# Kernel tuning notes

Hardware: AMD Instinct MI355X
Metric: run time of the kernel (lower is better)

## Reference

```python
import jax, jax.numpy as jnp
import numpy as np

L, E, K, H, I = 2, 8, 2, 1024, 2048  # stack_size, num_experts, top_k, hidden, intermediate
B, S = 1, 2048


def setup_inputs() -> dict:
    key = jax.random.key(0)
    k0, k1, k2, k3 = jax.random.split(key, 4)
    hidden_states = jax.random.normal(k0, (B, S, H), dtype=jnp.float32)
    router_w = jax.random.normal(k1, (L, H, E), dtype=jnp.float32) * 0.02
    gate_up_proj = jax.random.normal(k2, (L, E, H, 2 * I), dtype=jnp.float32) * (1.0 / np.sqrt(H))
    down_proj = jax.random.normal(k3, (L, E, I, H), dtype=jnp.float32) * (1.0 / np.sqrt(I))
    return {"hidden_states": hidden_states, "router_w": router_w,
            "gate_up_proj": gate_up_proj, "down_proj": down_proj}


def _moe_layer(x, rw, gu_w, dn_w):
    # x: [T,H]; one MoE block: RouterTopK(softmax) + full-capacity top-k GLU expert MLPs
    logits = x @ rw                                   # [T,E] router linear (fp32)
    aff = jax.nn.softmax(logits, axis=-1)
    vals, idx = jax.lax.top_k(aff, K)                 # [T,K]
    vals = vals / jnp.sum(vals, axis=-1, keepdims=True)  # normalize_top_k_affinities=True
    T = x.shape[0]
    # sparse combine weights [T,E]: normalized affinity on chosen experts, 0 elsewhere
    combine = jnp.zeros((T, E), x.dtype).at[jnp.arange(T)[:, None], idx].set(vals)
    gu = jnp.einsum('th,ehi->eti', x, gu_w)           # [E,T,2I] fused gate+up per expert
    gate, up = gu[..., :I], gu[..., I:]
    act = jax.nn.silu(gate) * up                      # GLU with silu
    eo = jnp.einsum('eti,eih->eth', act, dn_w)        # [E,T,H] down proj
    out = jnp.einsum('eth,te->th', eo, combine)       # combine over experts
    return out, logits


def reference(hidden_states, router_w, gate_up_proj, down_proj):
    Bx, Sx, Hx = hidden_states.shape
    x = hidden_states.reshape(-1, Hx)                 # [T,H]
    logits_all = []
    for l in range(L):                                # fixed small stack of layers
        x, logits = _moe_layer(x, router_w[l], gate_up_proj[l], down_proj[l])
        logits_all.append(logits)
    return x.reshape(Bx, Sx, Hx), jnp.stack(logits_all)  # output, [L,T,E] router logits
```

## Files before the change

kernel.cpp:

```cpp
#include <hip/hip_runtime.h>
#include <cstdint>
#include <cstddef>

constexpr int Lc = 2, Ec = 8, Hc = 1024, Ic = 2048, Tc = 2048;

typedef __bf16 bf16x8 __attribute__((ext_vector_type(8)));
typedef float f32x4 __attribute__((ext_vector_type(4)));

__device__ __forceinline__ unsigned short f2bf(float f) {
  unsigned u = __builtin_bit_cast(unsigned, f);
  u = (u + 0x7fffu + ((u >> 16) & 1u)) >> 16;
  return (unsigned short)u;
}
__device__ __forceinline__ float bf2f(unsigned short h) {
  unsigned u = (unsigned)h << 16;
  return __builtin_bit_cast(float, u);
}
__device__ __forceinline__ bf16x8 ldfrag(const unsigned short* p) {
  return __builtin_bit_cast(bf16x8, *(const uint4*)p);
}

template <bool WSPLIT>
__device__ __forceinline__ void wconv_block(const float* __restrict__ src,
                                            unsigned short* __restrict__ dh,
                                            unsigned short* __restrict__ dl,
                                            int K, int N, int idx, char* smem) {
  const int nN = N >> 6, nK = K >> 6;
  const int sN = 31 - __builtin_clz((unsigned)nN);
  const int sK = 31 - __builtin_clz((unsigned)nK);
  const int bx = idx & (nN - 1);
  const int by = (idx >> sN) & (nK - 1);
  const int e = idx >> (sN + sK);
  const int n0 = bx * 64, k0 = by * 64;
  const int NB = N >> 6, KS = K >> 5;
  src += (size_t)e * K * N;

  unsigned short(*lh)[66] = (unsigned short(*)[66])smem;
  unsigned short(*ll)[66] = (unsigned short(*)[66])(smem + 64 * 66 * 2);
  const int tid = threadIdx.x;

  {
    const int r = tid >> 2, cg = (tid & 3) * 16;
    const float* sp = src + (size_t)(k0 + r) * N + n0 + cg;
#pragma unroll
    for (int i = 0; i < 16; i += 4) {
      const float4 v = *(const float4*)(sp + i);
      const float f[4] = {v.x, v.y, v.z, v.w};
#pragma unroll
      for (int j = 0; j < 4; ++j) {
        const unsigned short h = f2bf(f[j]);
        lh[r][cg + i + j] = h;
        if constexpr (WSPLIT) ll[r][cg + i + j] = f2bf(f[j] - bf2f(h));
      }
    }
  }
  __syncthreads();
  {
    const int ksl = tid >> 7, q = (tid >> 5) & 3, n2 = (tid & 31) * 2;
    const int kb = ksl * 32 + q * 8;
    union { unsigned short s[16]; uint4 u[2]; } oh, ol;
#pragma unroll
    for (int s = 0; s < 2; ++s)
#pragma unroll
      for (int i = 0; i < 8; ++i) {
        oh.s[s * 8 + i] = lh[kb + i][n2 + s];
        if constexpr (WSPLIT) ol.s[s * 8 + i] = ll[kb + i][n2 + s];
      }
    const size_t cb =
        (((size_t)e * NB + (n0 >> 6)) * KS + (k0 >> 5) + ksl) * 2048 + q * 512 + n2 * 8;
    *(uint4*)(dh + cb) = oh.u[0];
    *(uint4*)(dh + cb + 8) = oh.u[1];
    if constexpr (WSPLIT) {
      *(uint4*)(dl + cb) = ol.u[0];
      *(uint4*)(dl + cb + 8) = ol.u[1];
    }
  }
}

template <bool WFUSE, bool WSPLIT>
__global__ __launch_bounds__(256) void router_kernel(
    const float* __restrict__ x, const float* __restrict__ rw, float* __restrict__ logits,
    unsigned short* __restrict__ xh, unsigned short* __restrict__ xl,
    const float* __restrict__ wsrc, unsigned short* __restrict__ wdh,
    unsigned short* __restrict__ wdl, int WK, int WN) {
  __shared__ __align__(16) char smem[WFUSE ? 16896 : 8192];
  const int bid = blockIdx.x;
  if constexpr (WFUSE) {
    if (bid >= Tc) {
      wconv_block<WSPLIT>(wsrc, wdh, wdl, WK, WN, bid - Tc, smem);
      return;
    }
  }
  float(*red)[Ec] = (float(*)[Ec])smem;
  const int t = bid;
  const int tid = threadIdx.x;
  const float* xr = x + (size_t)t * Hc;
  const int h0 = tid * 4;
  const float4 v = *(const float4*)(xr + h0);
  const float f[4] = {v.x, v.y, v.z, v.w};
  unsigned short hs[4], ls[4];
#pragma unroll
  for (int j = 0; j < 4; ++j) {
    hs[j] = f2bf(f[j]);
    ls[j] = f2bf(f[j] - bf2f(hs[j]));
  }
  *(uint2*)(xh + (size_t)t * Hc + h0) =
      uint2{(unsigned)hs[0] | ((unsigned)hs[1] << 16), (unsigned)hs[2] | ((unsigned)hs[3] << 16)};
  *(uint2*)(xl + (size_t)t * Hc + h0) =
      uint2{(unsigned)ls[0] | ((unsigned)ls[1] << 16), (unsigned)ls[2] | ((unsigned)ls[3] << 16)};

  float acc[Ec];
#pragma unroll
  for (int e = 0; e < Ec; ++e) acc[e] = 0.f;
#pragma unroll
  for (int j = 0; j < 4; ++j) {
    const float* w = rw + (size_t)(h0 + j) * Ec;
#pragma unroll
    for (int e = 0; e < Ec; ++e) acc[e] += f[j] * w[e];
  }
#pragma unroll
  for (int e = 0; e < Ec; ++e) red[tid][e] = acc[e];
  __syncthreads();
  for (int s = 128; s > 0; s >>= 1) {
    if (tid < s) {
#pragma unroll
      for (int e = 0; e < Ec; ++e) red[tid][e] += red[tid + s][e];
    }
    __syncthreads();
  }
  if (tid < Ec) logits[(size_t)t * Ec + tid] = red[0][tid];
}

__global__ void topk_kernel(const float* __restrict__ logits, int* __restrict__ cnt,
                            int* __restrict__ tokList, float* __restrict__ wList) {
  const int t = blockIdx.x * blockDim.x + threadIdx.x;
  if (t >= Tc) return;
  float l[Ec];
#pragma unroll
  for (int e = 0; e < Ec; ++e) l[e] = logits[(size_t)t * Ec + e];
  float b0 = -3.4e38f, b1 = -3.4e38f;
  int i0 = 0, i1 = 0;
#pragma unroll
  for (int e = 0; e < Ec; ++e) {
    if (l[e] > b0) { b1 = b0; i1 = i0; b0 = l[e]; i0 = e; }
    else if (l[e] > b1) { b1 = l[e]; i1 = e; }
  }
  const float w0 = 1.f / (1.f + expf(b1 - b0));
  const float w1 = 1.f - w0;
  int p0 = atomicAdd(&cnt[i0], 1);
  tokList[i0 * Tc + p0] = t;
  wList[i0 * Tc + p0] = w0;
  int p1 = atomicAdd(&cnt[i1], 1);
  tokList[i1 * Tc + p1] = t;
  wList[i1 * Tc + p1] = w1;
}

__global__ void offsets_kernel(const int* __restrict__ cnt, int* __restrict__ off) {
  if (threadIdx.x == 0) {
    int s = 0;
    for (int e = 0; e < Ec; ++e) { off[e] = s; s += cnt[e]; }
  }
}

template <bool SPLIT, bool WFUSE, bool WSPLIT>
__global__ __launch_bounds__(256, SPLIT ? 3 : 4) void gateup_kernel(
    const unsigned short* __restrict__ xh, const unsigned short* __restrict__ xl,
    const unsigned short* __restrict__ gwSh, const unsigned short* __restrict__ gwSl,
    const int* __restrict__ cnt, const int* __restrict__ off,
    const int* __restrict__ tokList, unsigned short* __restrict__ actH,
    unsigned short* __restrict__ actL, const float* __restrict__ wsrc,
    unsigned short* __restrict__ wdh, unsigned short* __restrict__ wdl, int WK, int WN) {
  constexpr int GB = 4096;
  __shared__ __align__(16) char smem[SPLIT ? 40960 : 20480];
  const int d = blockIdx.x;
  if constexpr (WFUSE) {
    if (d >= GB) {
      wconv_block<WSPLIT>(wsrc, wdh, wdl, WK, WN, d - GB, smem);
      return;
    }
  }
  const int lid = (d & 7) * (GB >> 3) + (d >> 3);
  const int mi = lid & 15;
  const int e = (lid >> 4) & 7;
  const int nb = lid >> 7;
  const int M = cnt[e];
  const int m0 = mi * 128;
  if (m0 >= M) return;
  const int tid = threadIdx.x;
  const int wv = tid >> 6, l64 = tid & 63;
  const int q = l64 >> 4, mr = l64 & 15;
  const int nc = wv * 16 + mr;

  unsigned short* sAh = (unsigned short*)smem;
  unsigned short* sAl = (unsigned short*)(SPLIT ? smem + 20480 : smem);

  const size_t fragoff = (size_t)(q * 64 + nc) * 8;
  const size_t gBase = (((size_t)e * 64 + nb) * 32) * 2048 + fragoff;
  const size_t uBase = (((size_t)e * 64 + nb + 32) * 32) * 2048 + fragoff;

  const int ar = tid >> 2, ak = (tid & 3) * 8;
  int r0 = m0 + ar;      if (r0 >= M) r0 = M - 1;
  int r1 = m0 + 64 + ar; if (r1 >= M) r1 = M - 1;
  const size_t a0o = (size_t)tokList[e * Tc + r0] * Hc + ak;
  const size_t a1o = (size_t)tokList[e * Tc + r1] * Hc + ak;

  f32x4 accg[8], accu[8];
#pragma unroll
  for (int i = 0; i < 8; ++i) {
    accg[i] = f32x4{0.f, 0.f, 0.f, 0.f};
    accu[i] = f32x4{0.f, 0.f, 0.f, 0.f};
  }

  uint4 paA0h{}, paA1h{}, paA0l{}, paA1l{};
  uint4 paB0h{}, paB1h{}, paB0l{}, paB1l{};
  bf16x8 bcAgh{}, bcAuh{}, bcAgl{}, bcAul{};
  bf16x8 bcBgh{}, bcBuh{}, bcBgl{}, bcBul{};

  paA0h = *(const uint4*)(xh + a0o);
  paA1h = *(const uint4*)(xh + a1o);
  if constexpr (SPLIT) {
    paA0l = *(const uint4*)(xl + a0o);
    paA1l = *(const uint4*)(xl + a1o);
  }
  *(uint4*)&sAh[ar * 40 + ak] = paA0h;
  *(uint4*)&sAh[(ar + 64) * 40 + ak] = paA1h;
  if constexpr (SPLIT) {
    *(uint4*)&sAl[ar * 40 + ak] = paA0l;
    *(uint4*)&sAl[(ar + 64) * 40 + ak] = paA1l;
  }
  bcAgh = ldfrag(gwSh + gBase);
  bcAuh = ldfrag(gwSh + uBase);
  if constexpr (SPLIT) {
    bcAgl = ldfrag(gwSl + gBase);
    bcAul = ldfrag(gwSl + uBase);
  }
  paA0h = *(const uint4*)(xh + a0o + 32);
  paA1h = *(const uint4*)(xh + a1o + 32);
  if constexpr (SPLIT) {
    paA0l = *(const uint4*)(xl + a0o + 32);
    paA1l = *(const uint4*)(xl + a1o + 32);
  }
  asm volatile("s_waitcnt lgkmcnt(0)" ::: "memory");
  __builtin_amdgcn_s_barrier();

#define GU_STEP(T, CUR, NX, PA0H, PA1H, PA0L, PA1L, PN0H, PN1H, PN0L, PN1L,             \
                BCGH, BCUH, BCGL, BCUL, BNGH, BNUH, BNGL, BNUL)                         \
  {                                                                                     \
    if ((T) + 1 < 32) {                                                                 \
      BNGH = ldfrag(gwSh + gBase + (size_t)((T) + 1) * 2048);                           \
      BNUH = ldfrag(gwSh + uBase + (size_t)((T) + 1) * 2048);                           \
      if constexpr (SPLIT) {                                                            \
        BNGL = ldfrag(gwSl + gBase + (size_t)((T) + 1) * 2048);                         \
        BNUL = ldfrag(gwSl + uBase + (size_t)((T) + 1) * 2048);                         \
      }                                                                                 \
    }                                                                                   \
    if ((T) + 2 < 32) {                                                                 \
      PN0H = *(const uint4*)(xh + a0o + ((T) + 2) * 32);                                \
      PN1H = *(const uint4*)(xh + a1o + ((T) + 2) * 32);                                \
      if constexpr (SPLIT) {                                                            \
        PN0L = *(const uint4*)(xl + a0o + ((T) + 2) * 32);                              \
        PN1L = *(const uint4*)(xl + a1o + ((T) + 2) * 32);                              \
      }                                                                                 \
    }                                                                                   \
    if ((T) + 1 < 32) {                                                                 \
      *(uint4*)&sAh[(NX) * 5120 + ar * 40 + ak] = PA0H;                                 \
      *(uint4*)&sAh[(NX) * 5120 + (ar + 64) * 40 + ak] = PA1H;                          \
      if constexpr (SPLIT) {                                                            \
        *(uint4*)&sAl[(NX) * 5120 + ar * 40 + ak] = PA0L;                               \
        *(uint4*)&sAl[(NX) * 5120 + (ar + 64) * 40 + ak] = PA1L;                        \
      }                                                                                 \
    }                                                                                   \
    __builtin_amdgcn_s_setprio(1);                                                      \
    _Pragma("unroll")                                                                   \
    for (int mt = 0; mt < 8; ++mt) {                                                    \
      const bf16x8 ah = ldfrag(&sAh[(CUR) * 5120 + (mt * 16 + mr) * 40 + q * 8]);       \
      accg[mt] = __builtin_amdgcn_mfma_f32_16x16x32_bf16(ah, BCGH, accg[mt], 0, 0, 0);  \
      accu[mt] = __builtin_amdgcn_mfma_f32_16x16x32_bf16(ah, BCUH, accu[mt], 0, 0, 0);  \
      if constexpr (SPLIT) {                                                            \
        const bf16x8 alr = ldfrag(&sAl[(CUR) * 5120 + (mt * 16 + mr) * 40 + q * 8]);    \
        accg[mt] = __builtin_amdgcn_mfma_f32_16x16x32_bf16(ah, BCGL, accg[mt], 0, 0, 0);\
        accg[mt] = __builtin_amdgcn_mfma_f32_16x16x32_bf16(alr, BCGH, accg[mt], 0, 0, 0);\
        accu[mt] = __builtin_amdgcn_mfma_f32_16x16x32_bf16(ah, BCUL, accu[mt], 0, 0, 0);\
        accu[mt] = __builtin_amdgcn_mfma_f32_16x16x32_bf16(alr, BCUH, accu[mt], 0, 0, 0);\
      }                                                                                 \
    }                                                                                   \
    __builtin_amdgcn_s_setprio(0);                                                      \
    if ((T) < 31) {                                                                     \
      asm volatile("s_waitcnt lgkmcnt(0)" ::: "memory");                                \
      __builtin_amdgcn_s_barrier();                                                     \
    }                                                                                   \
  }

  for (int t = 0; t < 32; t += 2) {
    GU_STEP(t, 0, 1, paA0h, paA1h, paA0l, paA1l, paB0h, paB1h, paB0l, paB1l,
            bcAgh, bcAuh, bcAgl, bcAul, bcBgh, bcBuh, bcBgl, bcBul)
    GU_STEP(t + 1, 1, 0, paB0h, paB1h, paB0l, paB1l, paA0h, paA1h, paA0l, paA1l,
            bcBgh, bcBuh, bcBgl, bcBul, bcAgh, bcAuh, bcAgl, bcAul)
  }
#undef GU_STEP

  const int valid = M - m0;
  const int rowbase = off[e] + m0;
#pragma unroll
  for (int mt = 0; mt < 8; ++mt) {
#pragma unroll
    for (int r = 0; r < 4; ++r) {
      const int row = mt * 16 + q * 4 + r;
      if (row < valid) {
        const float g = accg[mt][r];
        const float u = accu[mt][r];
        const float a = (g / (1.f + expf(-g))) * u;
        const size_t idx = (size_t)(rowbase + row) * Ic + (nb * 64 + nc);
        const unsigned short h = f2bf(a);
        actH[idx] = h;
        if constexpr (SPLIT) actL[idx] = f2bf(a - bf2f(h));
      }
    }
  }
}

template <bool SPLIT, bool WFUSE, bool WSPLIT>
__global__ __launch_bounds__(256, 4) void down_kernel(
    const unsigned short* __restrict__ actH, const unsigned short* __restrict__ actL,
    const unsigned short* __restrict__ dwSh, const unsigned short* __restrict__ dwSl,
    const int* __restrict__ cnt, const int* __restrict__ off,
    const int* __restrict__ tokList, const float* __restrict__ wList,
    float* __restrict__ out, const float* __restrict__ wsrc,
    unsigned short* __restrict__ wdh, unsigned short* __restrict__ wdl, int WK, int WN) {
  constexpr int GB = 2048;
  __shared__ __align__(16) char smem[SPLIT ? 40960 : 20480];
  __shared__ int sTok[128];
  __shared__ float sW[128];
  const int d = blockIdx.x;
  if constexpr (WFUSE) {
    if (d >= GB) {
      wconv_block<WSPLIT>(wsrc, wdh, wdl, WK, WN, d - GB, smem);
      return;
    }
  }
  const int lid = (d & 7) * (GB >> 3) + (d >> 3);
  const int mi = lid & 15;
  const int e = (lid >> 4) & 7;
  const int nb = lid >> 7;
  const int M = cnt[e];
  const int m0 = mi * 128;
  if (m0 >= M) return;
  const int tid = threadIdx.x;
  const int wv = tid >> 6, l64 = tid & 63;
  const int q = l64 >> 4, mr = l64 & 15;
  const int nc = wv * 16 + mr;

  unsigned short* sAh = (unsigned short*)smem;
  unsigned short* sAl = (unsigned short*)(SPLIT ? smem + 20480 : smem);

  if (tid < 128) {
    int r = m0 + tid;
    int rc = r < M ? r : M - 1;
    sTok[tid] = tokList[e * Tc + rc];
    sW[tid] = wList[e * Tc + rc];
  }

  const size_t fragoff = (size_t)(q * 64 + nc) * 8;
  const size_t bBase = (((size_t)e * 16 + nb) * 64) * 2048 + fragoff;
  const int offE = off[e];

  const int ar = tid >> 2, ak = (tid & 3) * 8;
  int r0 = m0 + ar;      if (r0 >= M) r0 = M - 1;
  int r1 = m0 + 64 + ar; if (r1 >= M) r1 = M - 1;
  const size_t a0o = (size_t)(offE + r0) * Ic + ak;
  const size_t a1o = (size_t)(offE + r1) * Ic + ak;

  f32x4 acc[8];
#pragma unroll
  for (int i = 0; i < 8; ++i) acc[i] = f32x4{0.f, 0.f, 0.f, 0.f};

  uint4 paA0h{}, paA1h{}, paA0l{}, paA1l{};
  uint4 paB0h{}, paB1h{}, paB0l{}, paB1l{};
  bf16x8 bcAh{}, bcAl{}, bcBh{}, bcBl{};

  paA0h = *(const uint4*)(actH + a0o);
  paA1h = *(const uint4*)(actH + a1o);
  if constexpr (SPLIT) {
    paA0l = *(const uint4*)(actL + a0o);
    paA1l = *(const uint4*)(actL + a1o);
  }
  *(uint4*)&sAh[ar * 40 + ak] = paA0h;
  *(uint4*)&sAh[(ar + 64) * 40 + ak] = paA1h;
  if constexpr (SPLIT) {
    *(uint4*)&sAl[ar * 40 + ak] = paA0l;
    *(uint4*)&sAl[(ar + 64) * 40 + ak] = paA1l;
  }
  bcAh = ldfrag(dwSh + bBase);
  if constexpr (SPLIT) bcAl = ldfrag(dwSl + bBase);
  paA0h = *(const uint4*)(actH + a0o + 32);
  paA1h = *(const uint4*)(actH + a1o + 32);
  if constexpr (SPLIT) {
    paA0l = *(const uint4*)(actL + a0o + 32);
    paA1l = *(const uint4*)(actL + a1o + 32);
  }
  asm volatile("s_waitcnt lgkmcnt(0)" ::: "memory");
  __builtin_amdgcn_s_barrier();

#define DN_STEP(T, CUR, NX, PA0H, PA1H, PA0L, PA1L, PN0H, PN1H, PN0L, PN1L,             \
                BCH, BCL, BNH, BNL)                                                     \
  {                                                                                     \
    if ((T) + 1 < 64) {                                                                 \
      BNH = ldfrag(dwSh + bBase + (size_t)((T) + 1) * 2048);                            \
      if constexpr (SPLIT) BNL = ldfrag(dwSl + bBase + (size_t)((T) + 1) * 2048);       \
    }                                                                                   \
    if ((T) + 2 < 64) {                                                                 \
      PN0H = *(const uint4*)(actH + a0o + ((T) + 2) * 32);                              \
      PN1H = *(const uint4*)(actH + a1o + ((T) + 2) * 32);                              \
      if constexpr (SPLIT) {                                                            \
        PN0L = *(const uint4*)(actL + a0o + ((T) + 2) * 32);                            \
        PN1L = *(const uint4*)(actL + a1o + ((T) + 2) * 32);                            \
      }                                                                                 \
    }                                                                                   \
    if ((T) + 1 < 64) {                                                                 \
      *(uint4*)&sAh[(NX) * 5120 + ar * 40 + ak] = PA0H;                                 \
      *(uint4*)&sAh[(NX) * 5120 + (ar + 64) * 40 + ak] = PA1H;                          \
      if constexpr (SPLIT) {                                                            \
        *(uint4*)&sAl[(NX) * 5120 + ar * 40 + ak] = PA0L;                               \
        *(uint4*)&sAl[(NX) * 5120 + (ar + 64) * 40 + ak] = PA1L;                        \
      }                                                                                 \
    }                                                                                   \
    __builtin_amdgcn_s_setprio(1);                                                      \
    _Pragma("unroll")                                                                   \
    for (int mt = 0; mt < 8; ++mt) {                                                    \
      const bf16x8 ah = ldfrag(&sAh[(CUR) * 5120 + (mt * 16 + mr) * 40 + q * 8]);       \
      acc[mt] = __builtin_amdgcn_mfma_f32_16x16x32_bf16(ah, BCH, acc[mt], 0, 0, 0);     \
      if constexpr (SPLIT) {                                                            \
        const bf16x8 alr = ldfrag(&sAl[(CUR) * 5120 + (mt * 16 + mr) * 40 + q * 8]);    \
        acc[mt] = __builtin_amdgcn_mfma_f32_16x16x32_bf16(ah, BCL, acc[mt], 0, 0, 0);   \
        acc[mt] = __builtin_amdgcn_mfma_f32_16x16x32_bf16(alr, BCH, acc[mt], 0, 0, 0);  \
      }                                                                                 \
    }                                                                                   \
    __builtin_amdgcn_s_setprio(0);                                                      \
    if ((T) < 63) {                                                                     \
      asm volatile("s_waitcnt lgkmcnt(0)" ::: "memory");                                \
      __builtin_amdgcn_s_barrier();                                                     \
    }                                                                                   \
  }

  for (int t = 0; t < 64; t += 2) {
    DN_STEP(t, 0, 1, paA0h, paA1h, paA0l, paA1l, paB0h, paB1h, paB0l, paB1l,
            bcAh, bcAl, bcBh, bcBl)
    DN_STEP(t + 1, 1, 0, paB0h, paB1h, paB0l, paB1l, paA0h, paA1h, paA0l, paA1l,
            bcBh, bcBl, bcAh, bcAl)
  }
#undef DN_STEP

  const int valid = M - m0;
#pragma unroll
  for (int mt = 0; mt < 8; ++mt) {
#pragma unroll
    for (int r = 0; r < 4; ++r) {
      const int row = mt * 16 + q * 4 + r;
      if (row < valid) {
        atomicAdd(&out[(size_t)sTok[row] * Hc + (nb * 64 + nc)], sW[row] * acc[mt][r]);
      }
    }
  }
}

extern "C" void kernel_launch(void* const* d_in, const int* in_sizes, int n_in, void* d_out,
                              int out_size, void* d_ws, size_t ws_size, hipStream_t stream) {
  const float* x_in = (const float*)d_in[0];
  const float* rw = (const float*)d_in[1];
  const float* guw = (const float*)d_in[2];
  const float* dnw = (const float*)d_in[3];
  float* out = (float*)d_out;
  float* logits_base = out + (size_t)Tc * Hc;

  uint8_t* w = (uint8_t*)d_ws;
  float* x1 = (float*)w;                    w += (size_t)Tc * Hc * 4;
  unsigned short* xh = (unsigned short*)w;  w += (size_t)Tc * Hc * 2;
  unsigned short* xl = (unsigned short*)w;  w += (size_t)Tc * Hc * 2;
  unsigned short* actH = (unsigned short*)w; w += (size_t)Tc * 2 * Ic * 2;
  unsigned short* actL = (unsigned short*)w; w += (size_t)Tc * 2 * Ic * 2;
  int* tokList = (int*)w;                   w += (size_t)Ec * Tc * 4;
  float* wList = (float*)w;                 w += (size_t)Ec * Tc * 4;
  int* cnt0 = (int*)w;                      w += 64;
  int* cnt1 = (int*)w;                      w += 64;
  int* off = (int*)w;                       w += 64;
  unsigned short* wAh = (unsigned short*)w; w += (size_t)Ec * 2 * Ic * Hc * 2;
  unsigned short* wAl = (unsigned short*)w; w += (size_t)Ec * 2 * Ic * Hc * 2;
  unsigned short* wBh = (unsigned short*)w; w += (size_t)Ec * Ic * Hc * 2;
  unsigned short* wBl = (unsigned short*)w; w += (size_t)Ec * Ic * Hc * 2;

  hipMemsetAsync(cnt0, 0, 192, stream);
  hipMemsetAsync(x1, 0, (size_t)Tc * Hc * 4, stream);
  hipMemsetAsync(out, 0, (size_t)Tc * Hc * 4, stream);

  const float* rw1 = rw + (size_t)Hc * Ec;
  const float* guw1 = guw + (size_t)Ec * Hc * 2 * Ic;
  const float* dnw1 = dnw + (size_t)Ec * Ic * Hc;

  router_kernel<true, true><<<Tc + 8192, 256, 0, stream>>>(x_in, rw, logits_base, xh, xl,
                                                           guw, wAh, wAl, Hc, 2 * Ic);
  topk_kernel<<<Tc / 256, 256, 0, stream>>>(logits_base, cnt0, tokList, wList);
  offsets_kernel<<<1, 64, 0, stream>>>(cnt0, off);
  gateup_kernel<true, true, true><<<4096 + 4096, 256, 0, stream>>>(
      xh, xl, wAh, wAl, cnt0, off, tokList, actH, actL, dnw, wBh, wBl, Ic, Hc);
  down_kernel<true, false, false><<<2048, 256, 0, stream>>>(
      actH, actL, wBh, wBl, cnt0, off, tokList, wList, x1, nullptr, nullptr, nullptr, 0, 0);

  router_kernel<true, false><<<Tc + 8192, 256, 0, stream>>>(
      x1, rw1, logits_base + (size_t)Tc * Ec, xh, xl, guw1, wAh, nullptr, Hc, 2 * Ic);
  topk_kernel<<<Tc / 256, 256, 0, stream>>>(logits_base + (size_t)Tc * Ec, cnt1, tokList, wList);
  offsets_kernel<<<1, 64, 0, stream>>>(cnt1, off);
  gateup_kernel<false, true, false><<<4096 + 4096, 256, 0, stream>>>(
      xh, xl, wAh, wAl, cnt1, off, tokList, actH, actL, dnw1, wBh, nullptr, Ic, Hc);
  down_kernel<false, false, false><<<2048, 256, 0, stream>>>(
      actH, actL, wBh, wBl, cnt1, off, tokList, wList, out, nullptr, nullptr, nullptr, 0, 0);
}
```

Measured before the change: 899.3 us.

## Load low-half activation fragments directly to registers and fuse layer-1 weight conversion into down kernel

In the split-precision gate-up and down kernels, the low-half activation tile is no longer staged through LDS. Each lane instead loads its own MFMA fragments straight from global memory into double-buffered registers, which removes LDS writes and reads and frees shared memory. The layer-1 gate-up weight conversion is moved from the layer-1 router launch into extra blocks of the layer-0 down kernel, so the weight conversion can overlap the down GEMM. The trade-offs are higher register pressure (down_kernel launch bounds drop to 3 waves) and uncoalesced global loads for the low-half activations.

```diff
diff --git a/kernel.cpp b/kernel.cpp
--- a/kernel.cpp
+++ b/kernel.cpp
@@ -171,7 +171,8 @@
     unsigned short* __restrict__ actL, const float* __restrict__ wsrc,
     unsigned short* __restrict__ wdh, unsigned short* __restrict__ wdl, int WK, int WN) {
   constexpr int GB = 4096;
-  __shared__ __align__(16) char smem[SPLIT ? 40960 : 20480];
+  constexpr int SMEMB = (WFUSE && WSPLIT) ? 33792 : 20480;
+  __shared__ __align__(16) char smem[SMEMB];
   const int d = blockIdx.x;
   if constexpr (WFUSE) {
     if (d >= GB) {
@@ -192,7 +193,6 @@
   const int nc = wv * 16 + mr;
 
   unsigned short* sAh = (unsigned short*)smem;
-  unsigned short* sAl = (unsigned short*)(SPLIT ? smem + 20480 : smem);
 
   const size_t fragoff = (size_t)(q * 64 + nc) * 8;
   const size_t gBase = (((size_t)e * 64 + nb) * 32) * 2048 + fragoff;
@@ -204,6 +204,16 @@
   const size_t a0o = (size_t)tokList[e * Tc + r0] * Hc + ak;
   const size_t a1o = (size_t)tokList[e * Tc + r1] * Hc + ak;
 
+  unsigned aoff[8];
+  if constexpr (SPLIT) {
+#pragma unroll
+    for (int mt = 0; mt < 8; ++mt) {
+      int r = m0 + mt * 16 + mr;
+      if (r >= M) r = M - 1;
+      aoff[mt] = (unsigned)tokList[e * Tc + r] * Hc + q * 8;
+    }
+  }
+
   f32x4 accg[8], accu[8];
 #pragma unroll
   for (int i = 0; i < 8; ++i) {
@@ -211,40 +221,31 @@
     accu[i] = f32x4{0.f, 0.f, 0.f, 0.f};
   }
 
-  uint4 paA0h{}, paA1h{}, paA0l{}, paA1l{};
-  uint4 paB0h{}, paB1h{}, paB0l{}, paB1l{};
+  uint4 paA0h{}, paA1h{};
+  uint4 paB0h{}, paB1h{};
   bf16x8 bcAgh{}, bcAuh{}, bcAgl{}, bcAul{};
   bf16x8 bcBgh{}, bcBuh{}, bcBgl{}, bcBul{};
+  bf16x8 alA[SPLIT ? 8 : 1], alB[SPLIT ? 8 : 1];
 
   paA0h = *(const uint4*)(xh + a0o);
   paA1h = *(const uint4*)(xh + a1o);
-  if constexpr (SPLIT) {
-    paA0l = *(const uint4*)(xl + a0o);
-    paA1l = *(const uint4*)(xl + a1o);
-  }
   *(uint4*)&sAh[ar * 40 + ak] = paA0h;
   *(uint4*)&sAh[(ar + 64) * 40 + ak] = paA1h;
-  if constexpr (SPLIT) {
-    *(uint4*)&sAl[ar * 40 + ak] = paA0l;
-    *(uint4*)&sAl[(ar + 64) * 40 + ak] = paA1l;
-  }
   bcAgh = ldfrag(gwSh + gBase);
   bcAuh = ldfrag(gwSh + uBase);
   if constexpr (SPLIT) {
     bcAgl = ldfrag(gwSl + gBase);
     bcAul = ldfrag(gwSl + uBase);
+#pragma unroll
+    for (int mt = 0; mt < 8; ++mt) alA[mt] = ldfrag(xl + aoff[mt]);
   }
   paA0h = *(const uint4*)(xh + a0o + 32);
   paA1h = *(const uint4*)(xh + a1o + 32);
-  if constexpr (SPLIT) {
-    paA0l = *(const uint4*)(xl + a0o + 32);
-    paA1l = *(const uint4*)(xl + a1o + 32);
-  }
   asm volatile("s_waitcnt lgkmcnt(0)" ::: "memory");
   __builtin_amdgcn_s_barrier();
 
-#define GU_STEP(T, CUR, NX, PA0H, PA1H, PA0L, PA1L, PN0H, PN1H, PN0L, PN1L,             \
-                BCGH, BCUH, BCGL, BCUL, BNGH, BNUH, BNGL, BNUL)                         \
+#define GU_STEP(T, CUR, NX, PA0H, PA1H, PN0H, PN1H,                                     \
+                BCGH, BCUH, BCGL, BCUL, BNGH, BNUH, BNGL, BNUL, ALC, ALN)               \
   {                                                                                     \
     if ((T) + 1 < 32) {                                                                 \
       BNGH = ldfrag(gwSh + gBase + (size_t)((T) + 1) * 2048);                           \
@@ -252,23 +253,18 @@
       if constexpr (SPLIT) {                                                            \
         BNGL = ldfrag(gwSl + gBase + (size_t)((T) + 1) * 2048);                         \
         BNUL = ldfrag(gwSl + uBase + (size_t)((T) + 1) * 2048);                         \
+        _Pragma("unroll")                                                               \
+        for (int mt = 0; mt < 8; ++mt)                                                  \
+          ALN[mt] = ldfrag(xl + aoff[mt] + ((T) + 1) * 32);                             \
       }                                                                                 \
     }                                                                                   \
     if ((T) + 2 < 32) {                                                                 \
       PN0H = *(const uint4*)(xh + a0o + ((T) + 2) * 32);                                \
       PN1H = *(const uint4*)(xh + a1o + ((T) + 2) * 32);                                \
-      if constexpr (SPLIT) {                                                            \
-        PN0L = *(const uint4*)(xl + a0o + ((T) + 2) * 32);                              \
-        PN1L = *(const uint4*)(xl + a1o + ((T) + 2) * 32);                              \
-      }                                                                                 \
     }                                                                                   \
     if ((T) + 1 < 32) {                                                                 \
       *(uint4*)&sAh[(NX) * 5120 + ar * 40 + ak] = PA0H;                                 \
       *(uint4*)&sAh[(NX) * 5120 + (ar + 64) * 40 + ak] = PA1H;                          \
-      if constexpr (SPLIT) {                                                            \
-        *(uint4*)&sAl[(NX) * 5120 + ar * 40 + ak] = PA0L;                               \
-        *(uint4*)&sAl[(NX) * 5120 + (ar + 64) * 40 + ak] = PA1L;                        \
-      }                                                                                 \
     }                                                                                   \
     __builtin_amdgcn_s_setprio(1);                                                      \
     _Pragma("unroll")                                                                   \
@@ -277,11 +273,10 @@
       accg[mt] = __builtin_amdgcn_mfma_f32_16x16x32_bf16(ah, BCGH, accg[mt], 0, 0, 0);  \
       accu[mt] = __builtin_amdgcn_mfma_f32_16x16x32_bf16(ah, BCUH, accu[mt], 0, 0, 0);  \
       if constexpr (SPLIT) {                                                            \
-        const bf16x8 alr = ldfrag(&sAl[(CUR) * 5120 + (mt * 16 + mr) * 40 + q * 8]);    \
         accg[mt] = __builtin_amdgcn_mfma_f32_16x16x32_bf16(ah, BCGL, accg[mt], 0, 0, 0);\
-        accg[mt] = __builtin_amdgcn_mfma_f32_16x16x32_bf16(alr, BCGH, accg[mt], 0, 0, 0);\
+        accg[mt] = __builtin_amdgcn_mfma_f32_16x16x32_bf16(ALC[mt], BCGH, accg[mt], 0, 0, 0);\
         accu[mt] = __builtin_amdgcn_mfma_f32_16x16x32_bf16(ah, BCUL, accu[mt], 0, 0, 0);\
-        accu[mt] = __builtin_amdgcn_mfma_f32_16x16x32_bf16(alr, BCUH, accu[mt], 0, 0, 0);\
+        accu[mt] = __builtin_amdgcn_mfma_f32_16x16x32_bf16(ALC[mt], BCUH, accu[mt], 0, 0, 0);\
       }                                                                                 \
     }                                                                                   \
     __builtin_amdgcn_s_setprio(0);                                                      \
@@ -292,10 +287,10 @@
   }
 
   for (int t = 0; t < 32; t += 2) {
-    GU_STEP(t, 0, 1, paA0h, paA1h, paA0l, paA1l, paB0h, paB1h, paB0l, paB1l,
-            bcAgh, bcAuh, bcAgl, bcAul, bcBgh, bcBuh, bcBgl, bcBul)
-    GU_STEP(t + 1, 1, 0, paB0h, paB1h, paB0l, paB1l, paA0h, paA1h, paA0l, paA1l,
-            bcBgh, bcBuh, bcBgl, bcBul, bcAgh, bcAuh, bcAgl, bcAul)
+    GU_STEP(t, 0, 1, paA0h, paA1h, paB0h, paB1h,
+            bcAgh, bcAuh, bcAgl, bcAul, bcBgh, bcBuh, bcBgl, bcBul, alA, alB)
+    GU_STEP(t + 1, 1, 0, paB0h, paB1h, paA0h, paA1h,
+            bcBgh, bcBuh, bcBgl, bcBul, bcAgh, bcAuh, bcAgl, bcAul, alB, alA)
   }
 #undef GU_STEP
 
@@ -320,7 +315,7 @@
 }
 
 template <bool SPLIT, bool WFUSE, bool WSPLIT>
-__global__ __launch_bounds__(256, 4) void down_kernel(
+__global__ __launch_bounds__(256, SPLIT ? 3 : 4) void down_kernel(
     const unsigned short* __restrict__ actH, const unsigned short* __restrict__ actL,
     const unsigned short* __restrict__ dwSh, const unsigned short* __restrict__ dwSl,
     const int* __restrict__ cnt, const int* __restrict__ off,
@@ -328,7 +323,7 @@
     float* __restrict__ out, const float* __restrict__ wsrc,
     unsigned short* __restrict__ wdh, unsigned short* __restrict__ wdl, int WK, int WN) {
   constexpr int GB = 2048;
-  __shared__ __align__(16) char smem[SPLIT ? 40960 : 20480];
+  __shared__ __align__(16) char smem[20480];
   __shared__ int sTok[128];
   __shared__ float sW[128];
   const int d = blockIdx.x;
@@ -351,7 +346,6 @@
   const int nc = wv * 16 + mr;
 
   unsigned short* sAh = (unsigned short*)smem;
-  unsigned short* sAl = (unsigned short*)(SPLIT ? smem + 20480 : smem);
 
   if (tid < 128) {
     int r = m0 + tid;
@@ -370,59 +364,58 @@
   const size_t a0o = (size_t)(offE + r0) * Ic + ak;
   const size_t a1o = (size_t)(offE + r1) * Ic + ak;
 
+  unsigned aoff[8];
+  if constexpr (SPLIT) {
+#pragma unroll
+    for (int mt = 0; mt < 8; ++mt) {
+      int r = m0 + mt * 16 + mr;
+      if (r >= M) r = M - 1;
+      aoff[mt] = (unsigned)(offE + r) * Ic + q * 8;
+    }
+  }
+
   f32x4 acc[8];
 #pragma unroll
   for (int i = 0; i < 8; ++i) acc[i] = f32x4{0.f, 0.f, 0.f, 0.f};
 
-  uint4 paA0h{}, paA1h{}, paA0l{}, paA1l{};
-  uint4 paB0h{}, paB1h{}, paB0l{}, paB1l{};
+  uint4 paA0h{}, paA1h{};
+  uint4 paB0h{}, paB1h{};
   bf16x8 bcAh{}, bcAl{}, bcBh{}, bcBl{};
+  bf16x8 alA[SPLIT ? 8 : 1], alB[SPLIT ? 8 : 1];
 
   paA0h = *(const uint4*)(actH + a0o);
   paA1h = *(const uint4*)(actH + a1o);
-  if constexpr (SPLIT) {
-    paA0l = *(const uint4*)(actL + a0o);
-    paA1l = *(const uint4*)(actL + a1o);
-  }
   *(uint4*)&sAh[ar * 40 + ak] = paA0h;
   *(uint4*)&sAh[(ar + 64) * 40 + ak] = paA1h;
+  bcAh = ldfrag(dwSh + bBase);
   if constexpr (SPLIT) {
-    *(uint4*)&sAl[ar * 40 + ak] = paA0l;
-    *(uint4*)&sAl[(ar + 64) * 40 + ak] = paA1l;
-  }
-  bcAh = ldfrag(dwSh + bBase);
-  if constexpr (SPLIT) bcAl = ldfrag(dwSl + bBase);
+    bcAl = ldfrag(dwSl + bBase);
+#pragma unroll
+    for (int mt = 0; mt < 8; ++mt) alA[mt] = ldfrag(actL + aoff[mt]);
+  }
   paA0h = *(const uint4*)(actH + a0o + 32);
   paA1h = *(const uint4*)(actH + a1o + 32);
-  if constexpr (SPLIT) {
-    paA0l = *(const uint4*)(actL + a0o + 32);
-    paA1l = *(const uint4*)(actL + a1o + 32);
-  }
   asm volatile("s_waitcnt lgkmcnt(0)" ::: "memory");
   __builtin_amdgcn_s_barrier();
 
-#define DN_STEP(T, CUR, NX, PA0H, PA1H, PA0L, PA1L, PN0H, PN1H, PN0L, PN1L,             \
-                BCH, BCL, BNH, BNL)                                                     \
+#define DN_STEP(T, CUR, NX, PA0H, PA1H, PN0H, PN1H, BCH, BCL, BNH, BNL, ALC, ALN)       \
   {                                                                                     \
     if ((T) + 1 < 64) {                                                                 \
       BNH = ldfrag(dwSh + bBase + (size_t)((T) + 1) * 2048);                            \
-      if constexpr (SPLIT) BNL = ldfrag(dwSl + bBase + (size_t)((T) + 1) * 2048);       \
+      if constexpr (SPLIT) {                                                            \
+        BNL = ldfrag(dwSl + bBase + (size_t)((T) + 1) * 2048);                          \
+        _Pragma("unroll")                                                               \
+        for (int mt = 0; mt < 8; ++mt)                                                  \
+          ALN[mt] = ldfrag(actL + aoff[mt] + ((T) + 1) * 32);                           \
+      }                                                                                 \
     }                                                                                   \
     if ((T) + 2 < 64) {                                                                 \
       PN0H = *(const uint4*)(actH + a0o + ((T) + 2) * 32);                              \
       PN1H = *(const uint4*)(actH + a1o + ((T) + 2) * 32);                              \
-      if constexpr (SPLIT) {                                                            \
-        PN0L = *(const uint4*)(actL + a0o + ((T) + 2) * 32);                            \
-        PN1L = *(const uint4*)(actL + a1o + ((T) + 2) * 32);                            \
-      }                                                                                 \
     }                                                                                   \
     if ((T) + 1 < 64) {                                                                 \
       *(uint4*)&sAh[(NX) * 5120 + ar * 40 + ak] = PA0H;                                 \
       *(uint4*)&sAh[(NX) * 5120 + (ar + 64) * 40 + ak] = PA1H;                          \
-      if constexpr (SPLIT) {                                                            \
-        *(uint4*)&sAl[(NX) * 5120 + ar * 40 + ak] = PA0L;                               \
-        *(uint4*)&sAl[(NX) * 5120 + (ar + 64) * 40 + ak] = PA1L;                        \
-      }                                                                                 \
     }                                                                                   \
     __builtin_amdgcn_s_setprio(1);                                                      \
     _Pragma("unroll")                                                                   \
@@ -430,9 +423,8 @@
       const bf16x8 ah = ldfrag(&sAh[(CUR) * 5120 + (mt * 16 + mr) * 40 + q * 8]);       \
       acc[mt] = __builtin_amdgcn_mfma_f32_16x16x32_bf16(ah, BCH, acc[mt], 0, 0, 0);     \
       if constexpr (SPLIT) {                                                            \
-        const bf16x8 alr = ldfrag(&sAl[(CUR) * 5120 + (mt * 16 + mr) * 40 + q * 8]);    \
         acc[mt] = __builtin_amdgcn_mfma_f32_16x16x32_bf16(ah, BCL, acc[mt], 0, 0, 0);   \
-        acc[mt] = __builtin_amdgcn_mfma_f32_16x16x32_bf16(alr, BCH, acc[mt], 0, 0, 0);  \
+        acc[mt] = __builtin_amdgcn_mfma_f32_16x16x32_bf16(ALC[mt], BCH, acc[mt], 0, 0, 0);\
       }                                                                                 \
     }                                                                                   \
     __builtin_amdgcn_s_setprio(0);                                                      \
@@ -443,10 +435,8 @@
   }
 
   for (int t = 0; t < 64; t += 2) {
-    DN_STEP(t, 0, 1, paA0h, paA1h, paA0l, paA1l, paB0h, paB1h, paB0l, paB1l,
-            bcAh, bcAl, bcBh, bcBl)
-    DN_STEP(t + 1, 1, 0, paB0h, paB1h, paB0l, paB1l, paA0h, paA1h, paA0l, paA1l,
-            bcBh, bcBl, bcAh, bcAl)
+    DN_STEP(t, 0, 1, paA0h, paA1h, paB0h, paB1h, bcAh, bcAl, bcBh, bcBl, alA, alB)
+    DN_STEP(t + 1, 1, 0, paB0h, paB1h, paA0h, paA1h, bcBh, bcBl, bcAh, bcAl, alB, alA)
   }
 #undef DN_STEP
 
@@ -502,11 +492,11 @@
   offsets_kernel<<<1, 64, 0, stream>>>(cnt0, off);
   gateup_kernel<true, true, true><<<4096 + 4096, 256, 0, stream>>>(
       xh, xl, wAh, wAl, cnt0, off, tokList, actH, actL, dnw, wBh, wBl, Ic, Hc);
-  down_kernel<true, false, false><<<2048, 256, 0, stream>>>(
-      actH, actL, wBh, wBl, cnt0, off, tokList, wList, x1, nullptr, nullptr, nullptr, 0, 0);
-
-  router_kernel<true, false><<<Tc + 8192, 256, 0, stream>>>(
-      x1, rw1, logits_base + (size_t)Tc * Ec, xh, xl, guw1, wAh, nullptr, Hc, 2 * Ic);
+  down_kernel<true, true, false><<<2048 + 8192, 256, 0, stream>>>(
+      actH, actL, wBh, wBl, cnt0, off, tokList, wList, x1, guw1, wAh, nullptr, Hc, 2 * Ic);
+
+  router_kernel<false, false><<<Tc, 256, 0, stream>>>(
+      x1, rw1, logits_base + (size_t)Tc * Ec, xh, xl, nullptr, nullptr, nullptr, 0, 0);
   topk_kernel<<<Tc / 256, 256, 0, stream>>>(logits_base + (size_t)Tc * Ec, cnt1, tokList, wList);
   offsets_kernel<<<1, 64, 0, stream>>>(cnt1, off);
   gateup_kernel<false, true, false><<<4096 + 4096, 256, 0, stream>>>(
```

Measured after the change: 1.472 ms. 63.7% more time.
